# Performance work log

Hardware: AMD Instinct MI355X
Metric: run time of the kernel (lower is better)

The kernel has to match this reference:

```python
import jax, jax.numpy as jnp
import numpy as np

TAU = 2.0
EPS_COH = 1e-8
EPS_NLL = 1e-7
ALPHA = 0.0
# component-vs-modality mask: rows = (common, synergy, g_spec, p_spec), cols = (gene, path)
MASK = np.array([[1.0, 1.0], [0.0, 0.0], [1.0, 0.0], [0.0, 1.0]], dtype=np.float32)


def l2norm(x, axis=-1):
    n = jnp.sqrt(jnp.sum(x * x, axis=axis, keepdims=True))
    return x / jnp.maximum(n, 1e-12)


def setup_inputs() -> dict:
    key = jax.random.key(0)
    ks = jax.random.split(key, 8)
    B, K, C, N = 64, 4, 256, 8192
    hazards = jax.random.uniform(ks[0], (B, K), dtype=jnp.float32)
    S = jnp.cumprod(1.0 - hazards, axis=1)  # survival curve, matches torch semantics
    indiv = jax.random.normal(ks[1], (B, 4, C), dtype=jnp.float32)
    gene = jax.random.normal(ks[2], (B, 1, C), dtype=jnp.float32)
    path = jax.random.normal(ks[3], (B, 1, C), dtype=jnp.float32)
    cohort_bank = jax.random.normal(ks[4], (K, N, 4, C), dtype=jnp.float32)
    label = jax.random.randint(ks[5], (B,), 0, K).astype(jnp.int32)
    c = jax.random.randint(ks[6], (B,), 0, 2).astype(jnp.int32)
    return {"hazards": hazards, "S": S, "indiv": indiv, "gene": gene,
            "path": path, "cohort_bank": cohort_bank, "label": label, "c": c}


def reference(hazards, S, indiv, gene, path, cohort_bank, label, c):
    B, K = hazards.shape
    dt = hazards.dtype
    # ---- NLLSurvLoss ----
    cf = c.astype(dt)[:, None]                       # [B,1] censoring flag
    Y = label.astype(jnp.int32)[:, None]             # [B,1]
    S_padded = jnp.concatenate([jnp.ones((B, 1), dt), S], axis=1)  # [B,K+1]
    s_y = jnp.take_along_axis(S_padded, Y, axis=1)
    h_y = jnp.take_along_axis(hazards, Y, axis=1)
    s_y1 = jnp.take_along_axis(S_padded, Y + 1, axis=1)
    clamp = lambda x: jnp.maximum(x, EPS_NLL)
    uncensored = -(1.0 - cf) * (jnp.log(clamp(s_y)) + jnp.log(clamp(h_y)))
    censored = -cf * jnp.log(clamp(s_y1))
    neg_l = censored + uncensored
    nll = ((1.0 - ALPHA) * neg_l + ALPHA * uncensored).mean()
    # ---- CohortLoss: intra ----
    indiv_n = l2norm(indiv)                          # [B,4,C]
    gp_n = l2norm(jnp.concatenate([gene, path], axis=1))  # [B,2,C]
    sim = jnp.einsum('bpc,btc->bpt', indiv_n, gp_n)  # [B,4,2]
    mask = jnp.asarray(MASK, dtype=dt)               # [4,2]
    intra = (jnp.abs(sim) * (1.0 - mask) - mask * sim).mean(axis=(1, 2)) + 1.0
    intra_loss = intra.mean()
    # ---- CohortLoss: inter (vectorized cohort-bank retrieval) ----
    n_cls, N = cohort_bank.shape[0], cohort_bank.shape[1]
    anchors = l2norm(indiv.mean(axis=1))             # [B,C]
    bank_means = cohort_bank.mean(axis=2)            # [n_cls,N,C]
    bank_n = l2norm(bank_means)                      # [n_cls,N,C]
    sims = jnp.einsum('knc,bc->bkn', bank_n, anchors)  # [B,n_cls,N]
    e = jnp.exp(sims / TAU)
    pos_mask = (label[:, None] == jnp.arange(n_cls, dtype=label.dtype)[None, :]).astype(dt)[:, :, None]  # [B,n_cls,1]
    ep = jnp.sum(e * pos_mask) / (B * N)                       # mean over B*N positive sims
    en = jnp.sum(e * (1.0 - pos_mask)) / (B * (n_cls - 1) * N)  # mean over B*(n_cls-1)*N negative sims
    inter_loss = -jnp.log((ep + EPS_COH) / (ep + en + EPS_COH))
    cohort_loss = intra_loss + inter_loss
    # Loss_factory: total = 1.0*nllsurv + 1.0*cohort
    return nll + cohort_loss
```

## Files before the change

### kernel.cpp

```cpp
#include <hip/hip_runtime.h>
#include <math.h>

#define BB 64
#define KK 4
#define CC 256
#define NN 8192
#define NROWS (KK*NN)
#define GRID_INTER 512
#define WPG 4
#define RPW 16
#define RPP 4
#define NPASS (RPW/RPP)

#define WS_A2_OFF    0
#define WS_SLOT_OFF  65536
#define WS_NLL_OFF   73728
#define WS_INTRA_OFF 73984
#define WS_TKT_OFF   74240

#define EPS_NLL 1e-7f

__device__ __forceinline__ float4 f4add(float4 a, float4 b){ return make_float4(a.x+b.x, a.y+b.y, a.z+b.z, a.w+b.w); }
__device__ __forceinline__ float4 f4scale(float4 a, float s){ return make_float4(a.x*s, a.y*s, a.z*s, a.w*s); }
__device__ __forceinline__ float dot4(float4 a, float4 b){ return a.x*b.x + a.y*b.y + a.z*b.z + a.w*b.w; }

__device__ __forceinline__ float wred(float v){
#pragma unroll
  for (int m = 32; m >= 1; m >>= 1) v += __shfl_xor(v, m, 64);
  return v;
}

__global__ __launch_bounds__(64) void prep_kernel(
    const float* __restrict__ hazards, const float* __restrict__ S,
    const float* __restrict__ indiv,   const float* __restrict__ gene,
    const float* __restrict__ path,    const int* __restrict__ label,
    const int* __restrict__ cvec,      char* __restrict__ ws)
{
  const int b = blockIdx.x;
  const int lane = threadIdx.x;

  const float4* ind4 = (const float4*)indiv + (size_t)b * 256;
  float4 i0 = ind4[  0 + lane];
  float4 i1 = ind4[ 64 + lane];
  float4 i2 = ind4[128 + lane];
  float4 i3 = ind4[192 + lane];
  float4 g  = ((const float4*)gene)[b*64 + lane];
  float4 p  = ((const float4*)path)[b*64 + lane];

  float4 am = f4scale(f4add(f4add(i0, i1), f4add(i2, i3)), 0.25f);
  float na = sqrtf(wred(dot4(am, am)));
  float4 an = f4scale(am, 1.0f / fmaxf(na, 1e-12f));
  ((float4*)(ws + WS_A2_OFF))[lane*64 + b] = an;

  float4 v[6] = {i0, i1, i2, i3, g, p};
#pragma unroll
  for (int j = 0; j < 6; ++j) {
    float n = sqrtf(wred(dot4(v[j], v[j])));
    v[j] = f4scale(v[j], 1.0f / fmaxf(n, 1e-12f));
  }

  float s[4][2];
#pragma unroll
  for (int pp = 0; pp < 4; ++pp)
#pragma unroll
    for (int t = 0; t < 2; ++t)
      s[pp][t] = wred(dot4(v[pp], v[4+t]));

  if (lane == 0) {
    float intra = (-s[0][0]) + (-s[0][1])
                + fabsf(s[1][0]) + fabsf(s[1][1])
                + (-s[2][0]) + fabsf(s[2][1])
                + fabsf(s[3][0]) + (-s[3][1]);
    intra = intra * 0.125f + 1.0f;
    ((float*)(ws + WS_INTRA_OFF))[b] = intra;

    int   Y  = label[b];
    float cf = (float)cvec[b];
    float s_y  = (Y == 0) ? 1.0f : S[b*KK + Y - 1];
    float s_y1 = S[b*KK + Y];
    float h_y  = hazards[b*KK + Y];
    float neg_l = -cf * logf(fmaxf(s_y1, EPS_NLL))
                  - (1.0f - cf) * (logf(fmaxf(s_y, EPS_NLL)) + logf(fmaxf(h_y, EPS_NLL)));
    ((float*)(ws + WS_NLL_OFF))[b] = neg_l;
  }
}

__global__ __launch_bounds__(256, 2) void inter_kernel(
    const float* __restrict__ bank, const int* __restrict__ label,
    char* __restrict__ ws, float* __restrict__ out)
{
  __shared__ float4 A2s[4096];
  __shared__ float4 bns[WPG][RPP][64];

  const int tid  = threadIdx.x;
  const int wave = tid >> 6;
  const int lane = tid & 63;

  const float4* A2g = (const float4*)(ws + WS_A2_OFF);
#pragma unroll
  for (int i = 0; i < 16; ++i) A2s[tid + i*256] = A2g[tid + i*256];
  __syncthreads();

  const int myLab = label[lane];
  const int gw    = blockIdx.x * WPG + wave;
  const int base  = gw * RPW;
  const int kk    = base >> 13;
  const bool ispos = (myLab == kk);
  const float4* bank4 = (const float4*)bank;

  float accE = 0.0f;

#pragma unroll 1
  for (int pass = 0; pass < NPASS; ++pass) {
    const int row0 = base + pass * RPP;

    float4 m[RPP];
#pragma unroll
    for (int r = 0; r < RPP; ++r) {
      const float4* rp = bank4 + (size_t)(row0 + r) * 256 + lane;
      float4 a0 = rp[0], a1 = rp[64], a2 = rp[128], a3 = rp[192];
      m[r] = f4scale(f4add(f4add(a0, a1), f4add(a2, a3)), 0.25f);
    }
#pragma unroll
    for (int r = 0; r < RPP; ++r) {
      float n = sqrtf(wred(dot4(m[r], m[r])));
      bns[wave][r][lane] = f4scale(m[r], 1.0f / fmaxf(n, 1e-12f));
    }

    float s0 = 0.0f, s1 = 0.0f, s2 = 0.0f, s3 = 0.0f;
#pragma unroll 8
    for (int cq = 0; cq < 64; ++cq) {
      float4 a = A2s[cq*64 + lane];
      s0 += dot4(a, bns[wave][0][cq]);
      s1 += dot4(a, bns[wave][1][cq]);
      s2 += dot4(a, bns[wave][2][cq]);
      s3 += dot4(a, bns[wave][3][cq]);
    }

    accE += expf(s0 * 0.5f) + expf(s1 * 0.5f)
          + expf(s2 * 0.5f) + expf(s3 * 0.5f);
  }

  float epf = ispos ? accE : 0.0f;
  float enf = ispos ? 0.0f : accE;

  epf = wred(epf);
  enf = wred(enf);
  if (lane == 0) {
    double* red = (double*)&bns[wave][0][0];
    red[0] = (double)epf;
    red[1] = (double)enf;
  }
  __syncthreads();

  double*   slots  = (double*)(ws + WS_SLOT_OFF);
  unsigned* ticket = (unsigned*)(ws + WS_TKT_OFF);
  volatile unsigned* tks = ((volatile unsigned*)&bns[0][0][0]) + 8;

  if (tid == 0) {
    double bep = 0.0, ben = 0.0;
#pragma unroll
    for (int w = 0; w < WPG; ++w) {
      double* rw = (double*)&bns[w][0][0];
      bep += rw[0]; ben += rw[1];
    }
    slots[blockIdx.x*2 + 0] = bep;
    slots[blockIdx.x*2 + 1] = ben;
    __threadfence();
    unsigned t = atomicAdd(ticket, 1u);
    *tks = t;
  }
  __syncthreads();

  if (*tks == GRID_INTER - 1 && wave == 0) {
    __threadfence();
    double pep = 0.0, pen = 0.0;
    for (int i = lane; i < GRID_INTER; i += 64) {
      pep += slots[2*i + 0];
      pen += slots[2*i + 1];
    }
#pragma unroll
    for (int m = 32; m >= 1; m >>= 1) {
      pep += __shfl_xor(pep, m, 64);
      pen += __shfl_xor(pen, m, 64);
    }
    float scal = ((const float*)(ws + WS_NLL_OFF))[lane]
               + ((const float*)(ws + WS_INTRA_OFF))[lane];
    scal = wred(scal);
    if (lane == 0) {
      double ep = pep / (double)(BB * NN);
      double en = pen / (double)(BB * (KK-1) * NN);
      double inter = -log((ep + 1e-8) / (ep + en + 1e-8));
      out[0] = (float)((double)scal / 64.0 + inter);
    }
  }
}

extern "C" void kernel_launch(void* const* d_in, const int* in_sizes, int n_in,
                              void* d_out, int out_size, void* d_ws, size_t ws_size,
                              hipStream_t stream)
{
  const float* hazards = (const float*)d_in[0];
  const float* S       = (const float*)d_in[1];
  const float* indiv   = (const float*)d_in[2];
  const float* gene    = (const float*)d_in[3];
  const float* path    = (const float*)d_in[4];
  const float* bank    = (const float*)d_in[5];
  const int*   label   = (const int*)d_in[6];
  const int*   cvec    = (const int*)d_in[7];
  char*  ws  = (char*)d_ws;
  float* out = (float*)d_out;

  hipMemsetAsync(ws + WS_TKT_OFF, 0, 4, stream);
  prep_kernel<<<dim3(BB), dim3(64), 0, stream>>>(hazards, S, indiv, gene, path, label, cvec, ws);
  inter_kernel<<<dim3(GRID_INTER), dim3(256), 0, stream>>>(bank, label, ws, out);
}
```

Before: 236.2 us.

## Broadcast normalized bank rows via readlane and use 512-thread blocks

Normalized bank-row vectors now stay in registers, and each lane's component is broadcast with readlane inside the dot-product loop. This replaces the per-wave shared-memory staging, and the LDS reads and writes that went with it, for the bank operand. Blocks grow to 8 waves, each handling 8 rows instead of 16, so the 64KB A2 tile in LDS is amortized over more waves per CU. The tradeoff is many scalar readlane operations (16 per cq iteration), which may serialize on SALU/VALU latency, and fewer rows per wave to amortize the A2 load.

```diff
diff --git a/kernel.cpp b/kernel.cpp
--- a/kernel.cpp
+++ b/kernel.cpp
@@ -7,8 +7,8 @@
 #define NN 8192
 #define NROWS (KK*NN)
 #define GRID_INTER 512
-#define WPG 4
-#define RPW 16
+#define WPG 8
+#define RPW 8
 #define RPP 4
 #define NPASS (RPW/RPP)
 
@@ -28,6 +28,10 @@
 #pragma unroll
   for (int m = 32; m >= 1; m >>= 1) v += __shfl_xor(v, m, 64);
   return v;
+}
+
+__device__ __forceinline__ float rl(float v, int l){
+  return __uint_as_float(__builtin_amdgcn_readlane(__float_as_uint(v), l));
 }
 
 __global__ __launch_bounds__(64) void prep_kernel(
@@ -85,12 +89,13 @@
   }
 }
 
-__global__ __launch_bounds__(256, 2) void inter_kernel(
+__global__ __launch_bounds__(512, 4) void inter_kernel(
     const float* __restrict__ bank, const int* __restrict__ label,
     char* __restrict__ ws, float* __restrict__ out)
 {
   __shared__ float4 A2s[4096];
-  __shared__ float4 bns[WPG][RPP][64];
+  __shared__ double redw[WPG][2];
+  __shared__ unsigned tkt_s;
 
   const int tid  = threadIdx.x;
   const int wave = tid >> 6;
@@ -98,7 +103,7 @@
 
   const float4* A2g = (const float4*)(ws + WS_A2_OFF);
 #pragma unroll
-  for (int i = 0; i < 16; ++i) A2s[tid + i*256] = A2g[tid + i*256];
+  for (int i = 0; i < 8; ++i) A2s[tid + i*512] = A2g[tid + i*512];
   __syncthreads();
 
   const int myLab = label[lane];
@@ -124,17 +129,17 @@
 #pragma unroll
     for (int r = 0; r < RPP; ++r) {
       float n = sqrtf(wred(dot4(m[r], m[r])));
-      bns[wave][r][lane] = f4scale(m[r], 1.0f / fmaxf(n, 1e-12f));
+      m[r] = f4scale(m[r], 1.0f / fmaxf(n, 1e-12f));
     }
 
     float s0 = 0.0f, s1 = 0.0f, s2 = 0.0f, s3 = 0.0f;
-#pragma unroll 8
+#pragma unroll 4
     for (int cq = 0; cq < 64; ++cq) {
       float4 a = A2s[cq*64 + lane];
-      s0 += dot4(a, bns[wave][0][cq]);
-      s1 += dot4(a, bns[wave][1][cq]);
-      s2 += dot4(a, bns[wave][2][cq]);
-      s3 += dot4(a, bns[wave][3][cq]);
+      s0 += a.x*rl(m[0].x,cq) + a.y*rl(m[0].y,cq) + a.z*rl(m[0].z,cq) + a.w*rl(m[0].w,cq);
+      s1 += a.x*rl(m[1].x,cq) + a.y*rl(m[1].y,cq) + a.z*rl(m[1].z,cq) + a.w*rl(m[1].w,cq);
+      s2 += a.x*rl(m[2].x,cq) + a.y*rl(m[2].y,cq) + a.z*rl(m[2].z,cq) + a.w*rl(m[2].w,cq);
+      s3 += a.x*rl(m[3].x,cq) + a.y*rl(m[3].y,cq) + a.z*rl(m[3].z,cq) + a.w*rl(m[3].w,cq);
     }
 
     accE += expf(s0 * 0.5f) + expf(s1 * 0.5f)
@@ -143,36 +148,29 @@
 
   float epf = ispos ? accE : 0.0f;
   float enf = ispos ? 0.0f : accE;
-
   epf = wred(epf);
   enf = wred(enf);
   if (lane == 0) {
-    double* red = (double*)&bns[wave][0][0];
-    red[0] = (double)epf;
-    red[1] = (double)enf;
+    redw[wave][0] = (double)epf;
+    redw[wave][1] = (double)enf;
   }
   __syncthreads();
 
   double*   slots  = (double*)(ws + WS_SLOT_OFF);
   unsigned* ticket = (unsigned*)(ws + WS_TKT_OFF);
-  volatile unsigned* tks = ((volatile unsigned*)&bns[0][0][0]) + 8;
 
   if (tid == 0) {
     double bep = 0.0, ben = 0.0;
 #pragma unroll
-    for (int w = 0; w < WPG; ++w) {
-      double* rw = (double*)&bns[w][0][0];
-      bep += rw[0]; ben += rw[1];
-    }
+    for (int w = 0; w < WPG; ++w) { bep += redw[w][0]; ben += redw[w][1]; }
     slots[blockIdx.x*2 + 0] = bep;
     slots[blockIdx.x*2 + 1] = ben;
     __threadfence();
-    unsigned t = atomicAdd(ticket, 1u);
-    *tks = t;
+    tkt_s = atomicAdd(ticket, 1u);
   }
   __syncthreads();
 
-  if (*tks == GRID_INTER - 1 && wave == 0) {
+  if (tkt_s == GRID_INTER - 1 && wave == 0) {
     __threadfence();
     double pep = 0.0, pen = 0.0;
     for (int i = lane; i < GRID_INTER; i += 64) {
@@ -213,5 +211,5 @@
 
   hipMemsetAsync(ws + WS_TKT_OFF, 0, 4, stream);
   prep_kernel<<<dim3(BB), dim3(64), 0, stream>>>(hazards, S, indiv, gene, path, label, cvec, ws);
-  inter_kernel<<<dim3(GRID_INTER), dim3(256), 0, stream>>>(bank, label, ws, out);
-}
+  inter_kernel<<<dim3(GRID_INTER), dim3(512), 0, stream>>>(bank, label, ws, out);
+}
```

Result: no change. 233.8 us (-1.0%).
